# Kernel tuning notes

Hardware: AMD Instinct MI355X
Metric: run time of the kernel (lower is better)

Reference implementation:

```python
import jax, jax.numpy as jnp
import numpy as np

D_MODEL = 1024
NUM_HEADS = 16
D_K = D_MODEL // NUM_HEADS


def setup_inputs() -> dict:
    key = jax.random.key(0)
    ks = jax.random.split(key, 16)
    B, S, D = 4, 2048, D_MODEL
    scale = 1.0 / np.sqrt(D)
    inp = {
        'Xs': jax.random.normal(ks[0], (B, S, D), jnp.float32),
        'Xt': jax.random.normal(ks[1], (B, S, D), jnp.float32),
    }
    names = ['qs', 'qt', 'ks', 'kt', 'vs', 'vt']
    for i, n in enumerate(names):
        inp['W_' + n] = jax.random.normal(ks[2 + 2 * i], (D, D), jnp.float32) * scale
        inp['b_' + n] = jax.random.normal(ks[3 + 2 * i], (D,), jnp.float32) * 0.01
    inp['attn_bias'] = jnp.zeros((1, 1, 1, 1), jnp.float32)
    return inp


def _split_heads(x):
    B, S, _ = x.shape
    return x.reshape(B, S, NUM_HEADS, D_K).transpose(0, 2, 1, 3)  # (B,H,S,dk)


def reference(Xs, Xt, W_qs, b_qs, W_qt, b_qt, W_ks, b_ks, W_kt, b_kt,
              W_vs, b_vs, W_vt, b_vt, attn_bias):
    # Dual-linear fused projections: Linear(x) = x @ W.T + b (torch convention)
    Q = Xs @ W_qs.T + b_qs + Xt @ W_qt.T + b_qt
    K = Xs @ W_ks.T + b_ks + Xt @ W_kt.T + b_kt
    V = Xs @ W_vs.T + b_vs + Xt @ W_vt.T + b_vt
    Q, K, V = _split_heads(Q), _split_heads(K), _split_heads(V)
    scores = jnp.einsum('bhqd,bhkd->bhqk', Q, K) / jnp.sqrt(jnp.float32(D_K))
    scores = scores + attn_bias  # scalar learned bias, broadcast
    probs = jax.nn.softmax(scores, axis=-1)
    out = jnp.einsum('bhqk,bhkd->bhqd', probs, V)  # (B,H,S,dk)
    B, H, S, dk = out.shape
    return out.transpose(0, 2, 1, 3).reshape(B, S, H * dk)
```

## Files before the change

### kernel.cpp

```cpp
#include <hip/hip_runtime.h>
#include <hip/hip_bf16.h>

typedef __bf16 bf16;
typedef __attribute__((ext_vector_type(8))) __bf16 bf16x8;
typedef __attribute__((ext_vector_type(4))) __bf16 bf16x4;
typedef __attribute__((ext_vector_type(4))) float f32x4;

#define D_MODEL 1024
#define NHEAD 16
#define DK 64
#define BB 4
#define SS 2048
#define MM 8192
#define KK 2048
#define NN 3072

#define LDP 72
#define QSCALE 0.18033688011112042f

__device__ __forceinline__ void glds16(const bf16* g, bf16* s) {
    __builtin_amdgcn_global_load_lds(
        (const __attribute__((address_space(1))) void*)g,
        (__attribute__((address_space(3))) void*)s, 16, 0, 0);
}

__device__ __forceinline__ void pack_chunk(const float* __restrict__ src,
                                           bf16* __restrict__ dst,
                                           int row_off, int col_off, int idx) {
    int m = idx >> 7;
    int cl = idx & 127;
    const float4* s4 = (const float4*)&src[((size_t)m << 10) + cl * 8];
    float4 v0 = s4[0], v1 = s4[1];
    bf16x8 o;
    o[0]=(bf16)v0.x; o[1]=(bf16)v0.y; o[2]=(bf16)v0.z; o[3]=(bf16)v0.w;
    o[4]=(bf16)v1.x; o[5]=(bf16)v1.y; o[6]=(bf16)v1.z; o[7]=(bf16)v1.w;
    int r = row_off + m;
    int k = col_off + cl * 8;
    int mi = r & 127, mt = r >> 7;
    int c = (k >> 3) & 7, kt = k >> 6;
    int slot = mi * 8 + (c ^ (mi & 7));
    *(bf16x8*)&dst[(((((size_t)mt * 32 + kt) << 10) + slot) << 3)] = o;
}

__global__ void pack_all(const float* __restrict__ Xs, const float* __restrict__ Xt,
                         const float* __restrict__ Wqs, const float* __restrict__ Wqt,
                         const float* __restrict__ Wks, const float* __restrict__ Wkt,
                         const float* __restrict__ Wvs, const float* __restrict__ Wvt,
                         const float* __restrict__ bqs, const float* __restrict__ bqt,
                         const float* __restrict__ bks, const float* __restrict__ bkt,
                         const float* __restrict__ bvs, const float* __restrict__ bvt,
                         bf16* __restrict__ Xp, bf16* __restrict__ Wp,
                         float* __restrict__ biasc) {
    int blk = blockIdx.x;
    if (blk < 8192) {
        int i = blk * 256 + threadIdx.x;
        int sel = i >> 20;
        int idx = i & 1048575;
        pack_chunk(sel ? Xt : Xs, Xp, 0, sel ? 1024 : 0, idx);
        return;
    }
    if (blk < 11264) {
        int i = (blk - 8192) * 256 + threadIdx.x;
        int gi = i >> 17;
        int idx = i & 131071;
        const float* src = (gi == 0) ? Wqs : (gi == 1) ? Wqt : (gi == 2) ? Wks
                         : (gi == 3) ? Wkt : (gi == 4) ? Wvs : Wvt;
        pack_chunk(src, Wp, (gi >> 1) * 1024, (gi & 1) * 1024, idx);
        return;
    }
    for (int n = threadIdx.x; n < NN; n += 256) {
        int g = n >> 10, c = n & 1023;
        const float* a = (g == 0) ? bqs : ((g == 1) ? bks : bvs);
        const float* b = (g == 0) ? bqt : ((g == 1) ? bkt : bvt);
        biasc[n] = a[c] + b[c];
    }
}

__global__ __launch_bounds__(256) void gemm_qkv(
    const bf16* __restrict__ Xp, const bf16* __restrict__ Wp,
    const float* __restrict__ biasc,
    bf16* __restrict__ Qb, bf16* __restrict__ Kb, bf16* __restrict__ Vt) {
    __shared__ __align__(16) bf16 sA[128 * 64];
    __shared__ __align__(16) bf16 sB[128 * 64];

    const int m0 = blockIdx.x * 128, n0 = blockIdx.y * 128;
    const int t = threadIdx.x, lane = t & 63, w = t >> 6;
    const int quad = lane >> 4, l16 = lane & 15, swz = l16 & 7;
    const int wm = (w >> 1) * 64, wn = (w & 1) * 64;

    f32x4 acc[4][4] = {};

    for (int ktI = 0; ktI < 32; ktI++) {
        const bf16* Ab = Xp + (((size_t)blockIdx.x * 32 + ktI) << 13);
        const bf16* Bb = Wp + (((size_t)blockIdx.y * 32 + ktI) << 13);
#pragma unroll
        for (int j = 0; j < 4; j++) {
            int u = (w * 4 + j) * 64 + lane;
            glds16(Ab + (size_t)u * 8, &sA[(w * 4 + j) * 512]);
            glds16(Bb + (size_t)u * 8, &sB[(w * 4 + j) * 512]);
        }
        __syncthreads();
#pragma unroll
        for (int kb = 0; kb < 2; kb++) {
            bf16x8 af[4], bfr[4];
#pragma unroll
            for (int mi = 0; mi < 4; mi++)
                af[mi] = *(const bf16x8*)&sA[(wm + mi * 16 + l16) * 64 + (((kb * 4 + quad) ^ swz) * 8)];
#pragma unroll
            for (int ni = 0; ni < 4; ni++)
                bfr[ni] = *(const bf16x8*)&sB[(wn + ni * 16 + l16) * 64 + (((kb * 4 + quad) ^ swz) * 8)];
#pragma unroll
            for (int mi = 0; mi < 4; mi++)
#pragma unroll
                for (int ni = 0; ni < 4; ni++)
                    acc[mi][ni] = __builtin_amdgcn_mfma_f32_16x16x32_bf16(
                        af[mi], bfr[ni], acc[mi][ni], 0, 0, 0);
        }
        __syncthreads();
    }

    const int g = n0 >> 10;
    for (int mi = 0; mi < 4; mi++) {
        int mbase = m0 + wm + mi * 16 + quad * 4;
        for (int ni = 0; ni < 4; ni++) {
            int n = n0 + wn + ni * 16 + l16;
            float bias = biasc[n];
            int c = n & 1023, h = c >> 6, d = c & 63;
            for (int r = 0; r < 4; r++) {
                int m = mbase + r;
                int b = m >> 11, s = m & 2047;
                size_t bh = (size_t)(b * NHEAD + h);
                float v = acc[mi][ni][r] + bias;
                if (g == 0)
                    Qb[(bh * SS + s) * DK + d] = (bf16)(v * QSCALE);
                else if (g == 1)
                    Kb[(bh * SS + s) * DK + d] = (bf16)v;
                else
                    Vt[(bh * DK + d) * SS + s] = (bf16)v;
            }
        }
    }
}

__global__ __launch_bounds__(256) void attn(
    const bf16* __restrict__ Qb, const bf16* __restrict__ Kb,
    const bf16* __restrict__ Vt, float* __restrict__ out) {
    __shared__ __align__(16) bf16 sK[64 * 64];
    __shared__ __align__(16) bf16 sV[64 * 64];
    __shared__ __align__(16) bf16 sP[4][32 * LDP];

    const int lid = blockIdx.x + gridDim.x * blockIdx.y;
    const int bh = (lid & 7) * 8 + ((lid >> 3) & 7);
    const int q0 = (lid >> 6) * 128;

    const int t = threadIdx.x;
    const int lane = t & 63, w = t >> 6;
    const int quad = lane >> 4, l16 = lane & 15, swz = l16 & 7;
    const int b = bh >> 4, h = bh & 15;

    const bf16* Qp = Qb + ((size_t)bh * SS + q0 + w * 32) * DK;
    bf16x8 qf[2][2];
#pragma unroll
    for (int f = 0; f < 2; f++)
#pragma unroll
        for (int kb = 0; kb < 2; kb++)
            qf[f][kb] = *(const bf16x8*)&Qp[(f * 16 + l16) * DK + kb * 32 + quad * 8];

    f32x4 o[2][4] = {};
    float lsum[2] = {0.f, 0.f};

    const bf16* Kp = Kb + (size_t)bh * SS * DK;
    const bf16* Vp = Vt + (size_t)bh * DK * SS;

    for (int kt = 0; kt < SS; kt += 64) {
#pragma unroll
        for (int j = 0; j < 2; j++) {
            int u = (w * 2 + j) * 64 + lane;
            int row = u >> 3;
            int cc = (u & 7) ^ (row & 7);
            glds16(Kp + (size_t)(kt + row) * DK + cc * 8, &sK[(w * 2 + j) * 512]);
            glds16(Vp + (size_t)row * SS + kt + cc * 8, &sV[(w * 2 + j) * 512]);
        }
        __syncthreads();

        f32x4 st[2][4] = {};
#pragma unroll
        for (int kb = 0; kb < 2; kb++)
#pragma unroll
            for (int ki = 0; ki < 4; ki++) {
                bf16x8 kf = *(const bf16x8*)&sK[(ki * 16 + l16) * 64 + (((kb * 4 + quad) ^ swz) * 8)];
                st[0][ki] = __builtin_amdgcn_mfma_f32_16x16x32_bf16(kf, qf[0][kb], st[0][ki], 0, 0, 0);
                st[1][ki] = __builtin_amdgcn_mfma_f32_16x16x32_bf16(kf, qf[1][kb], st[1][ki], 0, 0, 0);
            }

#pragma unroll
        for (int f = 0; f < 2; f++) {
            float ls = 0.f;
#pragma unroll
            for (int ki = 0; ki < 4; ki++) {
                float p0 = __builtin_amdgcn_exp2f(st[f][ki][0]);
                float p1 = __builtin_amdgcn_exp2f(st[f][ki][1]);
                float p2 = __builtin_amdgcn_exp2f(st[f][ki][2]);
                float p3 = __builtin_amdgcn_exp2f(st[f][ki][3]);
                ls += (p0 + p1) + (p2 + p3);
                bf16x4 pk;
                pk[0] = (bf16)p0; pk[1] = (bf16)p1; pk[2] = (bf16)p2; pk[3] = (bf16)p3;
                *(bf16x4*)&sP[w][(f * 16 + l16) * LDP + ki * 16 + quad * 4] = pk;
            }
            lsum[f] += ls;
        }

#pragma unroll
        for (int kb = 0; kb < 2; kb++) {
            bf16x8 af0 = *(const bf16x8*)&sP[w][(l16) * LDP + kb * 32 + quad * 8];
            bf16x8 af1 = *(const bf16x8*)&sP[w][(16 + l16) * LDP + kb * 32 + quad * 8];
#pragma unroll
            for (int ni = 0; ni < 4; ni++) {
                bf16x8 vf = *(const bf16x8*)&sV[(ni * 16 + l16) * 64 + (((kb * 4 + quad) ^ swz) * 8)];
                o[0][ni] = __builtin_amdgcn_mfma_f32_16x16x32_bf16(af0, vf, o[0][ni], 0, 0, 0);
                o[1][ni] = __builtin_amdgcn_mfma_f32_16x16x32_bf16(af1, vf, o[1][ni], 0, 0, 0);
            }
        }
        __syncthreads();
    }

#pragma unroll
    for (int f = 0; f < 2; f++) {
        lsum[f] += __shfl_xor(lsum[f], 16);
        lsum[f] += __shfl_xor(lsum[f], 32);
    }

    float* op = out + ((size_t)(b * SS + q0 + w * 32)) * D_MODEL + h * DK;
#pragma unroll
    for (int f = 0; f < 2; f++)
#pragma unroll
        for (int r = 0; r < 4; r++) {
            float linv = 1.0f / __shfl(lsum[f], quad * 4 + r);
#pragma unroll
            for (int ni = 0; ni < 4; ni++)
                op[(f * 16 + quad * 4 + r) * D_MODEL + ni * 16 + l16] = o[f][ni][r] * linv;
        }
}

extern "C" void kernel_launch(void* const* d_in, const int* in_sizes, int n_in,
                              void* d_out, int out_size, void* d_ws, size_t ws_size,
                              hipStream_t stream) {
    const float* Xs   = (const float*)d_in[0];
    const float* Xt   = (const float*)d_in[1];
    const float* Wqs  = (const float*)d_in[2];
    const float* bqs  = (const float*)d_in[3];
    const float* Wqt  = (const float*)d_in[4];
    const float* bqt  = (const float*)d_in[5];
    const float* Wks  = (const float*)d_in[6];
    const float* bks  = (const float*)d_in[7];
    const float* Wkt  = (const float*)d_in[8];
    const float* bkt  = (const float*)d_in[9];
    const float* Wvs  = (const float*)d_in[10];
    const float* bvs  = (const float*)d_in[11];
    const float* Wvt  = (const float*)d_in[12];
    const float* bvt  = (const float*)d_in[13];
    float* out = (float*)d_out;

    char* ws = (char*)d_ws;
    bf16*  Xp    = (bf16*)(ws);
    bf16*  Wp    = (bf16*)(ws + 33554432);
    float* biasc = (float*)(ws + 46137344);
    bf16*  Qb    = (bf16*)(ws + 46149632);
    bf16*  Kb    = (bf16*)(ws + 62926848);
    bf16*  Vt    = (bf16*)(ws + 79704064);

    pack_all<<<11265, 256, 0, stream>>>(Xs, Xt, Wqs, Wqt, Wks, Wkt, Wvs, Wvt,
                                        bqs, bqt, bks, bkt, bvs, bvt,
                                        Xp, Wp, biasc);

    gemm_qkv<<<dim3(MM / 128, NN / 128), 256, 0, stream>>>(Xp, Wp, biasc, Qb, Kb, Vt);

    attn<<<dim3(SS / 128, BB * NHEAD), 256, 0, stream>>>(Qb, Kb, Vt, out);
}
```

Measured before the change: 368.6 us.

## Rewrite QKV GEMM as 256x256 tile, 8-wave, double-buffered pipelined kernel

The QKV projection GEMM moves from 128x128 tiles with 4 waves and a single LDS buffer to 256x256 tiles with 8 waves. Global-to-LDS loads are double-buffered and prefetched two k-steps ahead. Each k-step is split into four MFMA quadrants interleaved with LDS fragment reads and staging, using explicit barriers, vmcnt waits and setprio. The aim is to hide memory latency and raise data reuse per tile, at the cost of 64KB of LDS, more accumulator registers, and a grid of only 384 blocks.

```diff
diff --git a/kernel.cpp b/kernel.cpp
--- a/kernel.cpp
+++ b/kernel.cpp
@@ -76,56 +76,152 @@
     }
 }
 
-__global__ __launch_bounds__(256) void gemm_qkv(
+#define VM8 asm volatile("s_waitcnt vmcnt(8)" ::: "memory")
+#define VM0 asm volatile("s_waitcnt vmcnt(0)" ::: "memory")
+#define VMNONE
+#define LGKM0 asm volatile("s_waitcnt lgkmcnt(0)" ::: "memory")
+
+#define STG(gsrc, ldst) do {                                                  \
+    glds16((gsrc) + ((size_t)t << 3), (ldst) + (w << 9));                     \
+    glds16((gsrc) + (((size_t)t + 512) << 3), (ldst) + ((w + 8) << 9));       \
+  } while (0)
+
+#define KSTEP(P, KT, DO_STAGE, VMOP) do {                                     \
+    const bf16* aP = &sA[P][aH][0];                                           \
+    const bf16* bP = &sB[P][bH][bR << 6];                                     \
+    bf16x8 aF0[4][2], aF1[4][2], bF0[2][2], bF1[2][2];                        \
+                                                       \
+    _Pragma("unroll")                                                         \
+    for (int mi = 0; mi < 4; mi++) {                                          \
+      aF0[mi][0] = *(const bf16x8*)&aP[((mi*16+l16)<<6) + ((quad^swz)<<3)];   \
+      aF0[mi][1] = *(const bf16x8*)&aP[((mi*16+l16)<<6) + (((4+quad)^swz)<<3)];\
+    }                                                                         \
+    _Pragma("unroll")                                                         \
+    for (int ni = 0; ni < 2; ni++) {                                          \
+      bF0[ni][0] = *(const bf16x8*)&bP[((ni*16+l16)<<6) + ((quad^swz)<<3)];   \
+      bF0[ni][1] = *(const bf16x8*)&bP[((ni*16+l16)<<6) + (((4+quad)^swz)<<3)];\
+    }                                                                         \
+    __builtin_amdgcn_s_barrier(); LGKM0;                                      \
+    __builtin_amdgcn_s_setprio(1);                                            \
+    _Pragma("unroll")                                                         \
+    for (int mi = 0; mi < 4; mi++)                                            \
+      _Pragma("unroll")                                                       \
+      for (int ni = 0; ni < 2; ni++) {                                        \
+        acc[mi][ni] = __builtin_amdgcn_mfma_f32_16x16x32_bf16(aF0[mi][0], bF0[ni][0], acc[mi][ni], 0,0,0); \
+        acc[mi][ni] = __builtin_amdgcn_mfma_f32_16x16x32_bf16(aF0[mi][1], bF0[ni][1], acc[mi][ni], 0,0,0); \
+      }                                                                       \
+    __builtin_amdgcn_s_setprio(0);                                            \
+    __builtin_amdgcn_s_barrier();                                             \
+                                                       \
+    _Pragma("unroll")                                                         \
+    for (int ni = 0; ni < 2; ni++) {                                          \
+      bF1[ni][0] = *(const bf16x8*)&bP[(((ni+2)*16+l16)<<6) + ((quad^swz)<<3)]; \
+      bF1[ni][1] = *(const bf16x8*)&bP[(((ni+2)*16+l16)<<6) + (((4+quad)^swz)<<3)]; \
+    }                                                                         \
+    __builtin_amdgcn_s_barrier(); LGKM0;                                      \
+    __builtin_amdgcn_s_setprio(1);                                            \
+    _Pragma("unroll")                                                         \
+    for (int mi = 0; mi < 4; mi++)                                            \
+      _Pragma("unroll")                                                       \
+      for (int ni = 0; ni < 2; ni++) {                                        \
+        acc[mi][ni+2] = __builtin_amdgcn_mfma_f32_16x16x32_bf16(aF0[mi][0], bF1[ni][0], acc[mi][ni+2], 0,0,0); \
+        acc[mi][ni+2] = __builtin_amdgcn_mfma_f32_16x16x32_bf16(aF0[mi][1], bF1[ni][1], acc[mi][ni+2], 0,0,0); \
+      }                                                                       \
+    __builtin_amdgcn_s_setprio(0);                                            \
+    __builtin_amdgcn_s_barrier();                                             \
+                                       \
+    _Pragma("unroll")                                                         \
+    for (int mi = 0; mi < 4; mi++) {                                          \
+      aF1[mi][0] = *(const bf16x8*)&aP[(((mi+4)*16+l16)<<6) + ((quad^swz)<<3)]; \
+      aF1[mi][1] = *(const bf16x8*)&aP[(((mi+4)*16+l16)<<6) + (((4+quad)^swz)<<3)]; \
+    }                                                                         \
+    if (DO_STAGE) {                                                           \
+      STG(Bg0 + ((size_t)((KT) + 2) << 13), &sB[P][0][0]);                    \
+      STG(Bg1 + ((size_t)((KT) + 2) << 13), &sB[P][1][0]);                    \
+    }                                                                         \
+    __builtin_amdgcn_s_barrier(); LGKM0;                                      \
+    __builtin_amdgcn_s_setprio(1);                                            \
+    _Pragma("unroll")                                                         \
+    for (int mi = 0; mi < 4; mi++)                                            \
+      _Pragma("unroll")                                                       \
+      for (int ni = 0; ni < 2; ni++) {                                        \
+        acc[mi+4][ni+2] = __builtin_amdgcn_mfma_f32_16x16x32_bf16(aF1[mi][0], bF1[ni][0], acc[mi+4][ni+2], 0,0,0); \
+        acc[mi+4][ni+2] = __builtin_amdgcn_mfma_f32_16x16x32_bf16(aF1[mi][1], bF1[ni][1], acc[mi+4][ni+2], 0,0,0); \
+      }                                                                       \
+    __builtin_amdgcn_s_setprio(0);                                            \
+    __builtin_amdgcn_s_barrier();                                             \
+                        \
+    if (DO_STAGE) {                                                           \
+      STG(Ag0 + ((size_t)((KT) + 2) << 13), &sA[P][0][0]);                    \
+      STG(Ag1 + ((size_t)((KT) + 2) << 13), &sA[P][1][0]);                    \
+    }                                                                         \
+    __builtin_amdgcn_s_barrier();                                             \
+    __builtin_amdgcn_s_setprio(1);                                            \
+    _Pragma("unroll")                                                         \
+    for (int mi = 0; mi < 4; mi++)                                            \
+      _Pragma("unroll")                                                       \
+      for (int ni = 0; ni < 2; ni++) {                                        \
+        acc[mi+4][ni] = __builtin_amdgcn_mfma_f32_16x16x32_bf16(aF1[mi][0], bF0[ni][0], acc[mi+4][ni], 0,0,0); \
+        acc[mi+4][ni] = __builtin_amdgcn_mfma_f32_16x16x32_bf16(aF1[mi][1], bF0[ni][1], acc[mi+4][ni], 0,0,0); \
+      }                                                                       \
+    __builtin_amdgcn_s_setprio(0);                                            \
+    VMOP;                                                                     \
+    __builtin_amdgcn_s_barrier();                                             \
+    __builtin_amdgcn_sched_barrier(0);                                        \
+  } while (0)
+
+__global__ __launch_bounds__(512, 2) void gemm_qkv(
     const bf16* __restrict__ Xp, const bf16* __restrict__ Wp,
     const float* __restrict__ biasc,
     bf16* __restrict__ Qb, bf16* __restrict__ Kb, bf16* __restrict__ Vt) {
-    __shared__ __align__(16) bf16 sA[128 * 64];
-    __shared__ __align__(16) bf16 sB[128 * 64];
-
-    const int m0 = blockIdx.x * 128, n0 = blockIdx.y * 128;
+    __shared__ __align__(16) bf16 sA[2][2][8192];
+    __shared__ __align__(16) bf16 sB[2][2][8192];
+
     const int t = threadIdx.x, lane = t & 63, w = t >> 6;
     const int quad = lane >> 4, l16 = lane & 15, swz = l16 & 7;
-    const int wm = (w >> 1) * 64, wn = (w & 1) * 64;
-
-    f32x4 acc[4][4] = {};
-
-    for (int ktI = 0; ktI < 32; ktI++) {
-        const bf16* Ab = Xp + (((size_t)blockIdx.x * 32 + ktI) << 13);
-        const bf16* Bb = Wp + (((size_t)blockIdx.y * 32 + ktI) << 13);
-#pragma unroll
-        for (int j = 0; j < 4; j++) {
-            int u = (w * 4 + j) * 64 + lane;
-            glds16(Ab + (size_t)u * 8, &sA[(w * 4 + j) * 512]);
-            glds16(Bb + (size_t)u * 8, &sB[(w * 4 + j) * 512]);
-        }
-        __syncthreads();
-#pragma unroll
-        for (int kb = 0; kb < 2; kb++) {
-            bf16x8 af[4], bfr[4];
-#pragma unroll
-            for (int mi = 0; mi < 4; mi++)
-                af[mi] = *(const bf16x8*)&sA[(wm + mi * 16 + l16) * 64 + (((kb * 4 + quad) ^ swz) * 8)];
-#pragma unroll
-            for (int ni = 0; ni < 4; ni++)
-                bfr[ni] = *(const bf16x8*)&sB[(wn + ni * 16 + l16) * 64 + (((kb * 4 + quad) ^ swz) * 8)];
-#pragma unroll
-            for (int mi = 0; mi < 4; mi++)
-#pragma unroll
-                for (int ni = 0; ni < 4; ni++)
-                    acc[mi][ni] = __builtin_amdgcn_mfma_f32_16x16x32_bf16(
-                        af[mi], bfr[ni], acc[mi][ni], 0, 0, 0);
-        }
-        __syncthreads();
-    }
-
-    const int g = n0 >> 10;
-    for (int mi = 0; mi < 4; mi++) {
-        int mbase = m0 + wm + mi * 16 + quad * 4;
+    const int wq = w & 3;
+    const int wm = (w >> 2) * 128;
+    const int wn = wq * 64;
+    const int aH = w >> 2;
+    const int bH = wq >> 1;
+    const int bR = (wq & 1) * 64;
+
+    const int bx = blockIdx.x, by = blockIdx.y;
+    const bf16* Ag0 = Xp + (((size_t)(bx * 2 + 0) * 32) << 13);
+    const bf16* Ag1 = Xp + (((size_t)(bx * 2 + 1) * 32) << 13);
+    const bf16* Bg0 = Wp + (((size_t)(by * 2 + 0) * 32) << 13);
+    const bf16* Bg1 = Wp + (((size_t)(by * 2 + 1) * 32) << 13);
+
+    f32x4 acc[8][4] = {};
+
+    STG(Ag0, &sA[0][0][0]); STG(Ag1, &sA[0][1][0]);
+    STG(Bg0, &sB[0][0][0]); STG(Bg1, &sB[0][1][0]);
+    STG(Ag0 + 8192, &sA[1][0][0]); STG(Ag1 + 8192, &sA[1][1][0]);
+    STG(Bg0 + 8192, &sB[1][0][0]); STG(Bg1 + 8192, &sB[1][1][0]);
+    VM8;
+    __builtin_amdgcn_s_barrier();
+    __builtin_amdgcn_sched_barrier(0);
+
+    int kt = 0;
+#pragma unroll 1
+    for (int i = 0; i < 15; i++, kt += 2) {
+        KSTEP(0, kt, 1, VM8);
+        KSTEP(1, kt + 1, 1, VM8);
+    }
+    KSTEP(0, 30, 0, VM0);
+    KSTEP(1, 31, 0, VMNONE);
+
+    const int g = by >> 2;
+    const int m00 = bx << 8, n00 = by << 8;
+#pragma unroll
+    for (int mi = 0; mi < 8; mi++) {
+        int mbase = m00 + wm + mi * 16 + quad * 4;
+#pragma unroll
         for (int ni = 0; ni < 4; ni++) {
-            int n = n0 + wn + ni * 16 + l16;
+            int n = n00 + wn + ni * 16 + l16;
             float bias = biasc[n];
             int c = n & 1023, h = c >> 6, d = c & 63;
+#pragma unroll
             for (int r = 0; r < 4; r++) {
                 int m = mbase + r;
                 int b = m >> 11, s = m & 2047;
@@ -273,7 +369,7 @@
                                         bqs, bqt, bks, bkt, bvs, bvt,
                                         Xp, Wp, biasc);
 
-    gemm_qkv<<<dim3(MM / 128, NN / 128), 256, 0, stream>>>(Xp, Wp, biasc, Qb, Kb, Vt);
+    gemm_qkv<<<dim3(MM / 256, NN / 256), 512, 0, stream>>>(Xp, Wp, biasc, Qb, Kb, Vt);
 
     attn<<<dim3(SS / 128, BB * NHEAD), 256, 0, stream>>>(Qb, Kb, Vt, out);
 }
```

After: 386.3 us. 4.8% more time.

## Enlarge QKV GEMM tile to 256x384 with double-buffered LDS prefetch

Applied to the files above, without the earlier changes.

The QKV projection GEMM now uses 768-thread blocks that each compute a 256x384 output tile, with every wave owning a 128x64 sub-tile. This raises operand reuse per LDS load and cuts global traffic. The next K-slice is prefetched into a second LDS buffer while MFMAs run on the current one, using explicit waitcnt, barriers and setprio to overlap loads with compute. The cost is very high LDS use (two 80 KB buffers) and many accumulator registers, which limits occupancy to one block per CU. The grid also shrinks to 256 blocks, which leaves a tail-balance risk.

```diff
diff --git a/kernel.cpp b/kernel.cpp
--- a/kernel.cpp
+++ b/kernel.cpp
@@ -76,57 +76,108 @@
     }
 }
 
-__global__ __launch_bounds__(256) void gemm_qkv(
+#define VM0 asm volatile("s_waitcnt vmcnt(0)" ::: "memory")
+#define LGKM0 asm volatile("s_waitcnt lgkmcnt(0)" ::: "memory")
+
+__global__ __launch_bounds__(768, 3) void gemm_qkv(
     const bf16* __restrict__ Xp, const bf16* __restrict__ Wp,
     const float* __restrict__ biasc,
     bf16* __restrict__ Qb, bf16* __restrict__ Kb, bf16* __restrict__ Vt) {
-    __shared__ __align__(16) bf16 sA[128 * 64];
-    __shared__ __align__(16) bf16 sB[128 * 64];
-
-    const int m0 = blockIdx.x * 128, n0 = blockIdx.y * 128;
+    __shared__ __align__(16) bf16 S[2][40960];
+
     const int t = threadIdx.x, lane = t & 63, w = t >> 6;
     const int quad = lane >> 4, l16 = lane & 15, swz = l16 & 7;
-    const int wm = (w >> 1) * 64, wn = (w & 1) * 64;
-
-    f32x4 acc[4][4] = {};
-
-    for (int ktI = 0; ktI < 32; ktI++) {
-        const bf16* Ab = Xp + (((size_t)blockIdx.x * 32 + ktI) << 13);
-        const bf16* Bb = Wp + (((size_t)blockIdx.y * 32 + ktI) << 13);
-#pragma unroll
-        for (int j = 0; j < 4; j++) {
-            int u = (w * 4 + j) * 64 + lane;
-            glds16(Ab + (size_t)u * 8, &sA[(w * 4 + j) * 512]);
-            glds16(Bb + (size_t)u * 8, &sB[(w * 4 + j) * 512]);
-        }
-        __syncthreads();
-#pragma unroll
-        for (int kb = 0; kb < 2; kb++) {
-            bf16x8 af[4], bfr[4];
-#pragma unroll
-            for (int mi = 0; mi < 4; mi++)
-                af[mi] = *(const bf16x8*)&sA[(wm + mi * 16 + l16) * 64 + (((kb * 4 + quad) ^ swz) * 8)];
-#pragma unroll
-            for (int ni = 0; ni < 4; ni++)
-                bfr[ni] = *(const bf16x8*)&sB[(wn + ni * 16 + l16) * 64 + (((kb * 4 + quad) ^ swz) * 8)];
-#pragma unroll
-            for (int mi = 0; mi < 4; mi++)
-#pragma unroll
-                for (int ni = 0; ni < 4; ni++)
+    const int wq = w % 6;
+    const int wm = (w / 6) * 128;
+    const int wn = wq * 64;
+    const int aOff = (w / 6) * 8192;
+    const int bOff = 16384 + (wq >> 1) * 8192 + (wq & 1) * 4096;
+
+    const int bx = blockIdx.x, by = blockIdx.y;
+
+    const bf16* gb[7];
+    int lo[7];
+#pragma unroll
+    for (int j = 0; j < 7; ++j) {
+        int idx = w + 12 * j;
+        if (idx < 32) {
+            int a0 = idx >> 4, woff = (idx & 15) * 512;
+            gb[j] = Xp + (((size_t)(bx * 2 + a0) * 32) << 13) + woff + lane * 8;
+            lo[j] = a0 * 8192 + woff;
+        } else if (idx < 80) {
+            int bi = idx - 32;
+            int b0 = bi >> 4, woff = (bi & 15) * 512;
+            gb[j] = Wp + (((size_t)(by * 3 + b0) * 32) << 13) + woff + lane * 8;
+            lo[j] = 16384 + b0 * 8192 + woff;
+        } else {
+            gb[j] = nullptr; lo[j] = 0;
+        }
+    }
+
+    f32x4 acc[8][4] = {};
+
+#pragma unroll
+    for (int j = 0; j < 7; ++j) {
+        int idx = w + 12 * j;
+        if (idx < 80) glds16(gb[j], &S[0][lo[j]]);
+    }
+    VM0;
+    __builtin_amdgcn_s_barrier();
+    __builtin_amdgcn_sched_barrier(0);
+
+#pragma unroll 1
+    for (int kt = 0; kt < 32; ++kt) {
+        bf16* Sc = &S[kt & 1][0];
+        bf16* Sn = &S[(kt & 1) ^ 1][0];
+        if (kt < 31) {
+#pragma unroll
+            for (int j = 0; j < 7; ++j) {
+                int idx = w + 12 * j;
+                if (idx < 80)
+                    glds16(gb[j] + ((size_t)(kt + 1) << 13), Sn + lo[j]);
+            }
+        }
+        const bf16* aP = Sc + aOff;
+        const bf16* bP = Sc + bOff;
+#pragma unroll
+        for (int kb = 0; kb < 2; ++kb) {
+            bf16x8 aF[8], bF[4];
+            const int sl = (((kb * 4 + quad) ^ swz) << 3);
+#pragma unroll
+            for (int mi = 0; mi < 8; ++mi)
+                aF[mi] = *(const bf16x8*)&aP[((mi * 16 + l16) << 6) + sl];
+#pragma unroll
+            for (int ni = 0; ni < 4; ++ni)
+                bF[ni] = *(const bf16x8*)&bP[((ni * 16 + l16) << 6) + sl];
+            __builtin_amdgcn_s_setprio(1);
+#pragma unroll
+            for (int mi = 0; mi < 8; ++mi)
+#pragma unroll
+                for (int ni = 0; ni < 4; ++ni)
                     acc[mi][ni] = __builtin_amdgcn_mfma_f32_16x16x32_bf16(
-                        af[mi], bfr[ni], acc[mi][ni], 0, 0, 0);
-        }
-        __syncthreads();
-    }
-
-    const int g = n0 >> 10;
-    for (int mi = 0; mi < 4; mi++) {
-        int mbase = m0 + wm + mi * 16 + quad * 4;
-        for (int ni = 0; ni < 4; ni++) {
-            int n = n0 + wn + ni * 16 + l16;
+                        aF[mi], bF[ni], acc[mi][ni], 0, 0, 0);
+            __builtin_amdgcn_s_setprio(0);
+        }
+        if (kt < 31) {
+            LGKM0;
+            VM0;
+            __builtin_amdgcn_s_barrier();
+            __builtin_amdgcn_sched_barrier(0);
+        }
+    }
+
+    const int m00 = bx << 8, n00 = by * 384;
+#pragma unroll
+    for (int mi = 0; mi < 8; ++mi) {
+        int mbase = m00 + wm + mi * 16 + quad * 4;
+#pragma unroll
+        for (int ni = 0; ni < 4; ++ni) {
+            int n = n00 + wn + ni * 16 + l16;
             float bias = biasc[n];
+            int g = n >> 10;
             int c = n & 1023, h = c >> 6, d = c & 63;
-            for (int r = 0; r < 4; r++) {
+#pragma unroll
+            for (int r = 0; r < 4; ++r) {
                 int m = mbase + r;
                 int b = m >> 11, s = m & 2047;
                 size_t bh = (size_t)(b * NHEAD + h);
@@ -273,7 +324,7 @@
                                         bqs, bqt, bks, bkt, bvs, bvt,
                                         Xp, Wp, biasc);
 
-    gemm_qkv<<<dim3(MM / 128, NN / 128), 256, 0, stream>>>(Xp, Wp, biasc, Qb, Kb, Vt);
+    gemm_qkv<<<dim3(MM / 256, NN / 384), 768, 0, stream>>>(Xp, Wp, biasc, Qb, Kb, Vt);
 
     attn<<<dim3(SS / 128, BB * NHEAD), 256, 0, stream>>>(Qb, Kb, Vt, out);
 }
```

New measurement: 623.0 us. 69.0% more time.
